# Optimization experiments

Measured on AMD Instinct MI355X. Metric: run time of the kernel, lower is better.

## Reference

```python
import jax, jax.numpy as jnp
import numpy as np

N, E = 30000, 240000          # nodes, edges per view
IN, D, OUT = 512, 128, 64      # in_dim, hidden_dim, out_dim
V, BLK, H, DM = 2, 2, 2, 64    # num_view, blk_size, num_heads, gate max-pool dim
NEG_ATT, NEG_OUT = 0.2, 0.01   # leaky_relu slopes (attention / outer)


def setup_inputs() -> dict:
    key = jax.random.key(0)
    ks = jax.random.split(key, 12)
    s = 0.05
    f32 = jnp.float32
    return {
        "ft": jax.random.normal(ks[0], (N, IN), f32),
        "src": jax.random.randint(ks[1], (V, E), 0, N, jnp.int32),
        "dst": jax.random.randint(ks[2], (V, E), 0, N, jnp.int32),
        "W_proj": jax.random.normal(ks[3], (IN, D), f32) * s,
        "W_embed": jax.random.normal(ks[4], (D, D), f32) * s,
        "a_l": jax.random.normal(ks[5], (V, BLK, H, D), f32) * s,
        "a_r": jax.random.normal(ks[6], (V, BLK, H, D), f32) * s,
        "Wv": jax.random.normal(ks[7], (V, BLK, H, D, D), f32) * s,
        "Wgm": jax.random.normal(ks[8], (V, BLK, D, DM), f32) * s,
        "Wgate": jax.random.normal(ks[9], (V, BLK, 2 * D + DM, H), f32) * s,
        "b_gate": jnp.zeros((V, BLK, H), f32),
        "W_tran": jax.random.normal(ks[10], (2 * D + DM and (D + V * H * D), OUT), f32) * s if False else jax.random.normal(ks[10], (D + V * H * D, OUT), f32) * s,
        "b_tran": jnp.zeros((OUT,), f32),
    }


def _seg_sum(x, idx):
    return jax.ops.segment_sum(x, idx, num_segments=N)


def _cgaan_layer(v, z, s_idx, d_idx, al, ar, wv, wgm, wgate, bg, merge):
    # v: [N,D] values, z: [N,D] attention features ('proj_z')
    # Multi-head attention logits: e_ij = leaky_relu(a_l.z_src + a_r.z_dst)  [E,H]
    logit_l = jnp.einsum("nd,hd->nh", z, al)
    logit_r = jnp.einsum("nd,hd->nh", z, ar)
    e = jax.nn.leaky_relu(logit_l[s_idx] + logit_r[d_idx], NEG_ATT)
    # edge softmax over incoming edges of each dst node
    m = jax.ops.segment_max(e, d_idx, num_segments=N)          # [N,H]
    ex = jnp.exp(e - m[d_idx])
    denom = _seg_sum(ex, d_idx)                                 # [N,H]
    alpha = ex / denom[d_idx]                                   # [E,H]
    # per-head value projection and weighted aggregation
    wvn = jnp.einsum("nd,hde->nhe", v, wv)                      # [N,H,D]
    agg = _seg_sum(alpha[:, :, None] * wvn[s_idx], d_idx)       # [N,H,D]
    # GaAN-style gate: sigmoid(FC([x_i, mean_j v_j, max_j (v_j Wgm)])) -> per-head scalar
    deg = _seg_sum(jnp.ones((s_idx.shape[0],), v.dtype), d_idx)  # [N]
    mean_n = _seg_sum(v[s_idx], d_idx) / jnp.maximum(deg, 1.0)[:, None]
    mx = jax.ops.segment_max((v @ wgm)[s_idx], d_idx, num_segments=N)
    mx = jnp.where(deg[:, None] > 0, mx, 0.0)                   # isolated nodes -> 0
    g = jax.nn.sigmoid(jnp.concatenate([v, mean_n, mx], -1) @ wgate + bg)  # [N,H]
    agg = g[:, :, None] * agg
    if merge == "mean":
        return agg.mean(axis=1)                                 # [N,D]
    return agg.reshape(agg.shape[0], -1)                        # cat -> [N,H*D]


def reference(ft, src, dst, W_proj, W_embed, a_l, a_r, Wv, Wgm, Wgate, b_gate, W_tran, b_tran):
    proj = ft @ W_proj                                          # [N,D]
    cur = [proj for _ in range(V)]
    for i in range(BLK):
        merge = "mean" if i < BLK - 1 else "cat"
        nxt = []
        for j in range(V):
            z = cur[j] @ W_embed
            h = _cgaan_layer(cur[j], z, src[j], dst[j], a_l[j, i], a_r[j, i],
                             Wv[j, i], Wgm[j, i], Wgate[j, i], b_gate[j, i], merge)
            nxt.append(jax.nn.leaky_relu(h, NEG_OUT))
        cur = nxt
    h = jnp.concatenate([proj] + cur, axis=-1)                  # [N, D+V*H*D]
    return h @ W_tran + b_tran
```

## Files before the change

### kernel.cpp

```cpp
#include <hip/hip_runtime.h>
#include <hip/hip_bf16.h>
#include <math.h>

#define NN 30000
#define EE 240000
#define IN_DIM 512
#define DD 128
#define OUTD 64
#define NV 2
#define NBLK 2
#define NH 2
#define DMM 64
#define NEG_ATT 0.2f
#define NEG_OUT 0.01f
#define CH 1024
#define NCH ((NN + CH - 1) / CH)

typedef __attribute__((ext_vector_type(8))) short bf16x8;
typedef __attribute__((ext_vector_type(4))) float f32x4;
typedef __attribute__((ext_vector_type(4))) unsigned short us4;
typedef __attribute__((ext_vector_type(8))) unsigned short us8;

#define OFF_PROJVM 0
#define OFF_WV     131072
#define OFF_WGM    262144
#define OFF_TRAN   278528
#define WT_TOTAL   319488

__device__ __forceinline__ unsigned short f2bf(float x) {
  unsigned u = __float_as_uint(x);
  return (unsigned short)((u + 0x7FFFu + ((u >> 16) & 1u)) >> 16);
}
__device__ __forceinline__ float bf2f(unsigned short u) {
  return __uint_as_float((unsigned)u << 16);
}
__device__ __forceinline__ void gload16(void* lds, const void* g) {
  __builtin_amdgcn_global_load_lds((const __attribute__((address_space(1))) unsigned int*)g,
                                   (__attribute__((address_space(3))) unsigned int*)lds, 16, 0, 0);
}

struct AUX {
  const int* fsrc; const int* fdst; const int* foff; int* fcur; int* fcsr;
  const unsigned short* lp0; const unsigned short* lp1; int lps;
  const float *lBl0, *lBr0, *lBl1, *lBr1, *lWg0, *lWg1;
  float4* llq; float2* llr;
};

__device__ void fill_body(int fb, int t, const AUX& a) {
  int e = fb * 256 + t;
  if (e >= NV * EE) return;
  int view = e / EE;
  int d = a.fdst[e];
  int p = atomicAdd(&a.fcur[view * NN + d], 1);
  a.fcsr[view * EE + a.foff[view * (NN + 1) + d] + p] = a.fsrc[e];
}

__device__ void llr_body(int lid, int t, const AUX& a) {
  int lane = t & 63, wid = t >> 6;
  int n = lid * 4 + wid;
  if (n >= NN) return;
  int k = lane * 2;
  unsigned av = *(const unsigned*)(a.lp0 + (size_t)n * a.lps + k);
  unsigned bv = *(const unsigned*)(a.lp1 + (size_t)n * a.lps + k);
  float ax = bf2f((unsigned short)av), ay = bf2f((unsigned short)(av >> 16));
  float bx = bf2f((unsigned short)bv), by = bf2f((unsigned short)(bv >> 16));
  float r[12];
  r[0]  = ax * a.lBl0[k * 2]     + ay * a.lBl0[k * 2 + 2];
  r[1]  = ax * a.lBl0[k * 2 + 1] + ay * a.lBl0[k * 2 + 3];
  r[2]  = ax * a.lBr0[k * 2]     + ay * a.lBr0[k * 2 + 2];
  r[3]  = ax * a.lBr0[k * 2 + 1] + ay * a.lBr0[k * 2 + 3];
  r[4]  = ax * a.lWg0[(128 + k) * 2]     + ay * a.lWg0[(129 + k) * 2];
  r[5]  = ax * a.lWg0[(128 + k) * 2 + 1] + ay * a.lWg0[(129 + k) * 2 + 1];
  r[6]  = bx * a.lBl1[k * 2]     + by * a.lBl1[k * 2 + 2];
  r[7]  = bx * a.lBl1[k * 2 + 1] + by * a.lBl1[k * 2 + 3];
  r[8]  = bx * a.lBr1[k * 2]     + by * a.lBr1[k * 2 + 2];
  r[9]  = bx * a.lBr1[k * 2 + 1] + by * a.lBr1[k * 2 + 3];
  r[10] = bx * a.lWg1[(128 + k) * 2]     + by * a.lWg1[(129 + k) * 2];
  r[11] = bx * a.lWg1[(128 + k) * 2 + 1] + by * a.lWg1[(129 + k) * 2 + 1];
  for (int s = 32; s; s >>= 1)
#pragma unroll
    for (int q = 0; q < 12; q++) r[q] += __shfl_xor(r[q], s);
  if (lane == 0) {
    a.llq[n] = make_float4(r[0], r[1], r[4], r[5]);
    a.llr[n] = make_float2(r[2], r[3]);
    a.llq[NN + n] = make_float4(r[6], r[7], r[10], r[11]);
    a.llr[NN + n] = make_float2(r[8], r[9]);
  }
}

__global__ __launch_bounds__(256) void kA_deg_prepw(const int* __restrict__ dst, int* __restrict__ deg,
                                                    const float* __restrict__ W_embed,
                                                    const float* __restrict__ a_l, const float* __restrict__ a_r,
                                                    const float* __restrict__ Wp, const float* __restrict__ Wgm,
                                                    float* __restrict__ Bl, float* __restrict__ Br,
                                                    float* __restrict__ wf) {
  int b = blockIdx.x;
  if (b < 1875) {
    int e = b * 256 + threadIdx.x;
    if (e < NV * EE) atomicAdd(&deg[(e / EE) * NN + dst[e]], 1);
    return;
  }
  int pb = b - 1875;
  if (pb < 256) {
    int idx = pb * 256 + threadIdx.x;
    int j = idx >> 15, k = (idx >> 6) & 511, n = idx & 63;
    const float* wp = Wp + (size_t)k * DD;
    const float* wg = Wgm + (size_t)(j * NBLK + 0) * DD * DMM + n;
    float s = 0.f;
    for (int e = 0; e < DD; e++) s += wp[e] * wg[(size_t)e * DMM];
    wf[idx] = s;
  } else {
    int idx = (pb - 256) * 256 + threadIdx.x;
    if (idx >= NV * NBLK * DD * NH) return;
    int h = idx & 1, dd = (idx >> 1) & 127, lv = idx >> 8;
    const float* w = W_embed + dd * DD;
    const float* al = a_l + (lv * NH + h) * DD;
    const float* ar = a_r + (lv * NH + h) * DD;
    float sl = 0.f, sr = 0.f;
    for (int e = 0; e < DD; e++) { float we = w[e]; sl += we * al[e]; sr += we * ar[e]; }
    Bl[idx] = sl; Br[idx] = sr;
  }
}

__global__ __launch_bounds__(256) void kB_scan1_wsplit(const int* __restrict__ deg, int* __restrict__ partial,
                                                       const float* __restrict__ Wp, const float* __restrict__ wf,
                                                       const float* __restrict__ Wv, const float* __restrict__ Wgm,
                                                       const float* __restrict__ Wt,
                                                       unsigned short* __restrict__ hi) {
  int b = blockIdx.x;
  if (b < 60) {
    int view = b / NCH, ch = b % NCH;
    const int* d = deg + view * NN + ch * CH;
    int rem = min(CH, NN - ch * CH);
    int t = threadIdx.x;
    int s = 0;
    for (int i = t; i < rem; i += 256) s += d[i];
    for (int k = 32; k; k >>= 1) s += __shfl_xor(s, k);
    __shared__ int wsum[4];
    if ((t & 63) == 0) wsum[t >> 6] = s;
    __syncthreads();
    if (t == 0) partial[b] = wsum[0] + wsum[1] + wsum[2] + wsum[3];
    return;
  }
  int wb = b - 60;
  const int pre[11] = {0, 256, 384, 512, 640, 768, 896, 1024, 1056, 1088, 1248};
  int y = 0;
  while (y < 10 && wb >= pre[y + 1]) y++;
  int bx = wb - pre[y];
  const float* src; int K, N; size_t doff;
  if (y == 0)      { src = Wp;                      K = 512; N = 128; doff = OFF_PROJVM; }
  else if (y <= 2) { int j = y - 1; src = wf + (size_t)j * 512 * 64; K = 512; N = 64; doff = OFF_PROJVM + (size_t)(128 + j * 64) * 512; }
  else if (y <= 6) { int lv = y - 3; src = Wv + (size_t)lv * 32768;  K = 256; N = 128; doff = OFF_WV + (size_t)lv * 32768; }
  else if (y <= 8) { int j = y - 7; src = Wgm + (size_t)(j * NBLK + 1) * 8192; K = 128; N = 64; doff = OFF_WGM + (size_t)j * 8192; }
  else             { src = Wt;                      K = 640; N = 64;  doff = OFF_TRAN; }
  int idx = bx * 256 + threadIdx.x;
  if (idx >= K * N) return;
  int n = idx / K, k = idx % K;
  int tk = k >> 6, g = (k >> 3) & 7, j2 = k & 7;
  int ks = (tk << 6) | ((g ^ (n & 7)) << 3) | j2;
  hi[doff + (size_t)n * K + ks] = f2bf(src[(size_t)k * N + n]);
}

__global__ __launch_bounds__(256) void k_scan3(const int* __restrict__ deg, const int* __restrict__ partial,
                                               int* __restrict__ off) {
  int b = blockIdx.x, view = b / NCH, ch = b % NCH;
  int coff = 0;
  for (int c = 0; c < ch; c++) coff += partial[view * NCH + c];
  int base = ch * CH;
  const int* d = deg + view * NN;
  int* o = off + view * (NN + 1);
  int t = threadIdx.x, lane = t & 63, w = t >> 6;
  int i0 = base + t * 4;
  int x0 = 0, x1 = 0, x2 = 0, x3 = 0;
  if (i0 + 3 < NN) { int4 q = *(const int4*)(d + i0); x0 = q.x; x1 = q.y; x2 = q.z; x3 = q.w; }
  else {
    if (i0     < NN) x0 = d[i0];
    if (i0 + 1 < NN) x1 = d[i0 + 1];
    if (i0 + 2 < NN) x2 = d[i0 + 2];
  }
  int tot = x0 + x1 + x2 + x3;
  int incl = tot;
  for (int k = 1; k < 64; k <<= 1) { int y = __shfl_up(incl, k); if (lane >= k) incl += y; }
  __shared__ int wt[4];
  if (lane == 63) wt[w] = incl;
  __syncthreads();
  int wexcl = 0;
  for (int k = 0; k < w; k++) wexcl += wt[k];
  int excl = coff + wexcl + incl - tot;
  if (i0     < NN) o[i0]     = excl;
  if (i0 + 1 < NN) o[i0 + 1] = excl + x0;
  if (i0 + 2 < NN) o[i0 + 2] = excl + x0 + x1;
  if (i0 + 3 < NN) o[i0 + 3] = excl + x0 + x1 + x2;
  if (ch == NCH - 1 && t == 0) o[NN] = coff + partial[b];
}

__global__ __launch_bounds__(256) void k_llr(AUX a) {
  llr_body(blockIdx.x, threadIdx.x, a);
}

__global__ __launch_bounds__(256) void k_edge(const int* __restrict__ off_, const int* __restrict__ csr_,
                                              const float4* __restrict__ lq_, const float2* __restrict__ lr_,
                                              const unsigned short* __restrict__ pk_, long viewStride,
                                              int ps, int vmoff0, int vmstep,
                                              const float* __restrict__ Wg_, const float* __restrict__ bg_,
                                              unsigned short* __restrict__ S_) {
  int view = blockIdx.y;
  const int* off = off_ + view * (NN + 1);
  const int* csr = csr_ + (size_t)view * EE;
  const float4* lq = lq_ + (size_t)view * NN;
  const float2* lrp = lr_ + (size_t)view * NN;
  const unsigned short* pk = pk_ + (size_t)view * viewStride;
  const char* pkc = (const char*)pk;
  int psb = ps * 2;
  int vmb = (vmoff0 + view * vmstep) * 2;
  const float* Wg = Wg_ + (size_t)view * NBLK * (2 * DD + DMM) * NH;
  const float* bg = bg_ + view * NBLK * NH;
  unsigned short* S = S_ + (size_t)view * NN * 256;

  int lane = threadIdx.x & 63, wid = threadIdx.x >> 6;
  int n = blockIdx.x * 4 + wid;
  int e0 = off[n], nb = off[n + 1] - e0;
  int half = lane >> 5, hl = lane & 31;
  if (nb == 0) {
    us4 z4 = {0, 0, 0, 0};
    *(us4*)(S + (size_t)n * 256 + half * 128 + 4 * hl) = z4;
    return;
  }
  float2 lrn = lrp[n];
  int voff = 8 * hl;
  int moff = vmb + 4 * hl;
  float sa0[4] = {0.f, 0.f, 0.f, 0.f}, sa1[4] = {0.f, 0.f, 0.f, 0.f};
  float d0 = 0.f, d1 = 0.f, tm0 = 0.f, tm1 = 0.f, vm0 = -INFINITY, vm1 = -INFINITY;
  for (int base = 0; base < nb; base += 64) {
    int i = base + lane;
    float w0 = 0.f, w1 = 0.f; unsigned boff = 0;
    if (i < nb) {
      int sidx = csr[e0 + i];
      boff = (unsigned)(sidx * psb);
      float4 qq = lq[sidx];
      float x0 = qq.x + lrn.x, x1 = qq.y + lrn.y;
      x0 = (x0 > 0.f) ? x0 : NEG_ATT * x0;
      x1 = (x1 > 0.f) ? x1 : NEG_ATT * x1;
      w0 = __expf(x0); w1 = __expf(x1);
      d0 += w0; d1 += w1; tm0 += qq.z; tm1 += qq.w;
    }
    int cnt = min(64, nb - base);
    int steps = (cnt + 1) >> 1;
    int j = half;
    unsigned bo = __shfl(boff, j);
    float wa = __shfl(w0, j), wb = __shfl(w1, j);
    us4 vq = *(const us4*)(pkc + bo + voff);
    unsigned mu = *(const unsigned*)(pkc + bo + moff);
    bool ok = (j < cnt);
    for (int s = 0; s < steps; s++) {
      int j1 = 2 * (s + 1) + half;
      int jc = min(j1, 63);
      unsigned bo1 = __shfl(boff, jc);
      float wa1 = __shfl(w0, jc), wb1 = __shfl(w1, jc);
      us4 vq1 = *(const us4*)(pkc + bo1 + voff);
      unsigned mu1 = *(const unsigned*)(pkc + bo1 + moff);
      float v0 = bf2f(vq[0]), v1 = bf2f(vq[1]), v2 = bf2f(vq[2]), v3 = bf2f(vq[3]);
      sa0[0] += wa * v0; sa0[1] += wa * v1; sa0[2] += wa * v2; sa0[3] += wa * v3;
      sa1[0] += wb * v0; sa1[1] += wb * v1; sa1[2] += wb * v2; sa1[3] += wb * v3;
      float mv0 = ok ? bf2f((unsigned short)mu) : -INFINITY;
      float mv1 = ok ? bf2f((unsigned short)(mu >> 16)) : -INFINITY;
      vm0 = fmaxf(vm0, mv0); vm1 = fmaxf(vm1, mv1);
      vq = vq1; mu = mu1; wa = wa1; wb = wb1; ok = (j1 < cnt);
    }
  }
#pragma unroll
  for (int k = 0; k < 4; k++) {
    sa0[k] += __shfl_xor(sa0[k], 32);
    sa1[k] += __shfl_xor(sa1[k], 32);
  }
  vm0 = fmaxf(vm0, __shfl_xor(vm0, 32));
  vm1 = fmaxf(vm1, __shfl_xor(vm1, 32));
  for (int s = 32; s; s >>= 1) { d0 += __shfl_xor(d0, s); d1 += __shfl_xor(d1, s); }
  unsigned vnu = *(const unsigned*)(pk + (size_t)n * ps + 2 * lane);
  float vnx = bf2f((unsigned short)vnu), vny = bf2f((unsigned short)(vnu >> 16));
  float im = 1.f / (float)nb;
  float p0 = vnx * Wg[(2 * lane) * 2]     + vny * Wg[(2 * lane + 1) * 2]     + tm0 * im;
  float p1 = vnx * Wg[(2 * lane) * 2 + 1] + vny * Wg[(2 * lane + 1) * 2 + 1] + tm1 * im;
  if (half == 1) {
    p0 += vm0 * Wg[(256 + 2 * hl) * 2]     + vm1 * Wg[(256 + 2 * hl + 1) * 2];
    p1 += vm0 * Wg[(256 + 2 * hl) * 2 + 1] + vm1 * Wg[(256 + 2 * hl + 1) * 2 + 1];
  }
  for (int s = 32; s; s >>= 1) { p0 += __shfl_xor(p0, s); p1 += __shfl_xor(p1, s); }
  float g0 = 1.f / (1.f + __expf(-(p0 + bg[0])));
  float g1 = 1.f / (1.f + __expf(-(p1 + bg[1])));
  float q0 = g0 / d0, q1 = g1 / d1;
  us4 o4;
  if (half == 0) {
    o4[0] = f2bf(sa0[0] * q0); o4[1] = f2bf(sa0[1] * q0);
    o4[2] = f2bf(sa0[2] * q0); o4[3] = f2bf(sa0[3] * q0);
  } else {
    o4[0] = f2bf(sa1[0] * q1); o4[1] = f2bf(sa1[1] * q1);
    o4[2] = f2bf(sa1[2] * q1); o4[3] = f2bf(sa1[3] * q1);
  }
  *(us4*)(S + (size_t)n * 256 + half * 128 + 4 * hl) = o4;
}

struct GB {
  const void* A[4];
  unsigned long long bofs[4];
  float* C[4];
  unsigned short* P[4];
  int ldc[4];
  int pldc[4];
};

template <int BN, int BM, bool ABF>
__global__ __launch_bounds__(256) void gemm_mfma(
    GB gb, AUX aux, const unsigned short* __restrict__ Bth,
    int lda, int ldb, int M, int K,
    const float* __restrict__ bias, float fs, int flags) {
  constexpr int NSUB = BN / 32;
  constexpr int CPW = BN / 32;
  constexpr int MS = BM / 32;
  __shared__ __align__(16) unsigned short Ah[BM][64];
  __shared__ __align__(16) unsigned short Bh[BN][64];
  int xb = blockIdx.x;
  const int z = blockIdx.z;
  if (flags & 8) {
    if (xb < 938) { fill_body(xb + 938 * z, threadIdx.x, aux); return; }
    xb -= 938;
  }
  if (flags & 16) {
    if (xb < 3750) { llr_body(xb + 3750 * z, threadIdx.x, aux); return; }
    xb -= 3750;
  }
  const float* __restrict__ Af = (const float*)gb.A[z];
  const unsigned short* __restrict__ Ab = (const unsigned short*)gb.A[z];
  float* __restrict__ C = gb.C[z];
  unsigned short* __restrict__ P = gb.P[z];
  const int ldc = gb.ldc[z], pldc = gb.pldc[z];
  const size_t bofs = gb.bofs[z];
  const int t = threadIdx.x;
  const int lane = t & 63, wv = t >> 6;
  const int lm = lane & 15, lg = lane >> 4;
  const int m0w = (wv & 1) * (BM / 2), n0w = (wv >> 1) * (BN / 2);
  const int row0 = xb * BM;
  f32x4 acc[MS][NSUB];
#pragma unroll
  for (int ms = 0; ms < MS; ms++)
#pragma unroll
    for (int ns = 0; ns < NSUB; ns++) acc[ms][ns] = (f32x4)0.f;

  float4 apre[MS][2];
  const int ar_ = t >> 3, ag_ = t & 7;

  auto loadA = [&](int k0) {
    if constexpr (!ABF) {
#pragma unroll
      for (int q = 0; q < MS; q++) {
        int rr = row0 + q * 32 + ar_;
        if (rr < M) {
          const float* p = Af + (size_t)rr * lda + k0 + ag_ * 8;
          apre[q][0] = *(const float4*)p;
          apre[q][1] = *(const float4*)(p + 4);
        } else {
          apre[q][0] = make_float4(0.f, 0.f, 0.f, 0.f);
          apre[q][1] = make_float4(0.f, 0.f, 0.f, 0.f);
        }
      }
    }
  };
  auto storeA = [&]() {
    if constexpr (!ABF) {
#pragma unroll
      for (int q = 0; q < MS; q++) {
        int r = q * 32 + ar_;
        us8 h8;
        float vals[8] = {apre[q][0].x, apre[q][0].y, apre[q][0].z, apre[q][0].w,
                         apre[q][1].x, apre[q][1].y, apre[q][1].z, apre[q][1].w};
#pragma unroll
        for (int e = 0; e < 8; e++) h8[e] = f2bf(vals[e]);
        int c = (ag_ ^ (r & 7)) << 3;
        *(us8*)&Ah[r][c] = h8;
      }
    }
  };
  auto stageA_bf = [&](int k0) {
    if constexpr (ABF) {
#pragma unroll
      for (int q = 0; q < MS; q++) {
        int r = q * 32 + ar_;
        int rr = min(row0 + r, M - 1);
        int scg = ag_ ^ (r & 7);
        gload16((char*)&Ah[0][0] + q * 4096 + t * 16,
                Ab + (size_t)rr * lda + k0 + scg * 8);
      }
    }
  };
  auto stageB = [&](int k0) {
#pragma unroll
    for (int q = 0; q < CPW; q++) {
      int chunk = wv * CPW + q;
      int o = chunk * 1024 + lane * 16;
      int n = o >> 7;
      int pq = (o >> 4) & 7;
      size_t gofs = bofs + (size_t)n * ldb + k0 + pq * 8;
      gload16((char*)&Bh[0][0] + o, Bth + gofs);
    }
  };

  loadA(0);
  for (int k0 = 0; k0 < K; k0 += 64) {
    if constexpr (ABF) stageA_bf(k0); else storeA();
    stageB(k0);
    __syncthreads();
    if constexpr (!ABF) { if (k0 + 64 < K) loadA(k0 + 64); }
#pragma unroll
    for (int kc = 0; kc < 2; kc++) {
      bf16x8 afh[MS], bfh[NSUB];
#pragma unroll
      for (int ms = 0; ms < MS; ms++) {
        int R = m0w + ms * 16 + lm;
        int c = (((kc * 4 + lg) ^ (R & 7)) << 3);
        afh[ms] = *(const bf16x8*)&Ah[R][c];
      }
#pragma unroll
      for (int ns = 0; ns < NSUB; ns++) {
        int R = n0w + ns * 16 + lm;
        int c = (((kc * 4 + lg) ^ (R & 7)) << 3);
        bfh[ns] = *(const bf16x8*)&Bh[R][c];
      }
#pragma unroll
      for (int ms = 0; ms < MS; ms++)
#pragma unroll
        for (int ns = 0; ns < NSUB; ns++)
          acc[ms][ns] = __builtin_amdgcn_mfma_f32_16x16x32_bf16(afh[ms], bfh[ns], acc[ms][ns], 0, 0, 0);
    }
    __syncthreads();
  }
#pragma unroll
  for (int ms = 0; ms < MS; ms++)
#pragma unroll
    for (int ns = 0; ns < NSUB; ns++)
#pragma unroll
      for (int j = 0; j < 4; j++) {
        int row = row0 + m0w + ms * 16 + lg * 4 + j;
        if (row >= M) continue;
        int col = n0w + ns * 16 + lm;
        float val = acc[ms][ns][j] * fs;
        if (bias) val += bias[col];
        if (flags & 2) val = (val > 0.f) ? val : NEG_OUT * val;
        if (C) C[(size_t)row * ldc + col] = val;
        if (P) P[(size_t)row * pldc + col] = f2bf(val);
      }
}

extern "C" void kernel_launch(void* const* d_in, const int* in_sizes, int n_in,
                              void* d_out, int out_size, void* d_ws, size_t ws_size,
                              hipStream_t stream) {
  const float* ft      = (const float*)d_in[0];
  const int*   src     = (const int*)  d_in[1];
  const int*   dst     = (const int*)  d_in[2];
  const float* W_proj  = (const float*)d_in[3];
  const float* W_embed = (const float*)d_in[4];
  const float* a_l     = (const float*)d_in[5];
  const float* a_r     = (const float*)d_in[6];
  const float* Wv      = (const float*)d_in[7];
  const float* Wgm     = (const float*)d_in[8];
  const float* Wgate   = (const float*)d_in[9];
  const float* b_gate  = (const float*)d_in[10];
  const float* W_tran  = (const float*)d_in[11];
  const float* b_tran  = (const float*)d_in[12];
  float* out = (float*)d_out;
  char* ws = (char*)d_ws;
  (void)in_sizes; (void)n_in; (void)out_size; (void)ws_size;

  size_t o = 0;
  auto take = [&](size_t bytes) { size_t r = o; o += (bytes + 255) & ~(size_t)255; return r; };
  int*   deg     = (int*)(ws + take((size_t)NV * NN * 4));
  int*   cursor  = (int*)(ws + take((size_t)NV * NN * 4));
  int*   csr_off = (int*)(ws + take((size_t)NV * (NN + 1) * 4));
  int*   csr_src = (int*)(ws + take((size_t)NV * EE * 4));
  int*   partial = (int*)(ws + take((size_t)NV * NCH * 4));
  float* Bl      = (float*)(ws + take((size_t)NV * NBLK * DD * NH * 4));
  float* Br      = (float*)(ws + take((size_t)NV * NBLK * DD * NH * 4));
  float* wf      = (float*)(ws + take((size_t)NV * 512 * 64 * 4));
  unsigned short* whi = (unsigned short*)(ws + take((size_t)WT_TOTAL * 2));
  float* h       = (float*)(ws + take((size_t)NN * 640 * 4));
  unsigned short* pk0 = (unsigned short*)(ws + take((size_t)NN * 256 * 2));
  unsigned short* pk1 = (unsigned short*)(ws + take((size_t)NV * NN * 192 * 2));
  unsigned short* Sbf = (unsigned short*)(ws + take((size_t)NV * NN * 256 * 2));
  float4* lqb    = (float4*)(ws + take((size_t)NV * NN * 16));
  float2* lrb    = (float2*)(ws + take((size_t)NV * NN * 8));

  const int HSTR = 640;
  const int GMB = (NN + 127) / 128;

  hipMemsetAsync(deg, 0, (size_t)(((size_t)NV * NN * 4 + 255) & ~(size_t)255) + (size_t)NV * NN * 4, stream);
  kA_deg_prepw<<<2135, 256, 0, stream>>>(dst, deg, W_embed, a_l, a_r, W_proj, Wgm, Bl, Br, wf);
  kB_scan1_wsplit<<<1308, 256, 0, stream>>>(deg, partial, W_proj, wf, Wv, Wgm, W_tran, whi);
  k_scan3<<<NV * NCH, 256, 0, stream>>>(deg, partial, csr_off);

  {
    GB gb = {};
    gb.A[0] = ft; gb.A[1] = ft;
    gb.bofs[0] = OFF_PROJVM; gb.bofs[1] = OFF_PROJVM + (size_t)128 * 512;
    gb.C[0] = h;  gb.ldc[0] = HSTR;
    gb.P[0] = pk0;       gb.pldc[0] = 256;
    gb.P[1] = pk0 + 128; gb.pldc[1] = 256;
    AUX ax = {};
    ax.fsrc = src; ax.fdst = dst; ax.foff = csr_off; ax.fcur = cursor; ax.fcsr = csr_src;
    gemm_mfma<128, 128, false><<<dim3(938 + GMB, 1, 2), 256, 0, stream>>>(gb, ax, whi, IN_DIM, 512,
                                                                          NN, 512, nullptr, 1.f, 8);
  }

  {
    AUX ax = {};
    ax.lp0 = pk0; ax.lp1 = pk0; ax.lps = 256;
    ax.lBl0 = Bl + 0 * 256; ax.lBr0 = Br + 0 * 256;
    ax.lBl1 = Bl + 2 * 256; ax.lBr1 = Br + 2 * 256;
    ax.lWg0 = Wgate; ax.lWg1 = Wgate + (size_t)NBLK * 320 * NH;
    ax.llq = lqb; ax.llr = lrb;
    k_llr<<<NN / 4, 256, 0, stream>>>(ax);
  }
  k_edge<<<dim3(NN / 4, 2), 256, 0, stream>>>(csr_off, csr_src, lqb, lrb,
                                              pk0, 0L, 256, 128, 64,
                                              Wgate, b_gate, Sbf);
  {
    GB gb = {};
    for (int j = 0; j < 2; j++) {
      gb.A[j] = Sbf + (size_t)j * NN * 256;
      gb.bofs[j] = OFF_WV + (size_t)(j * 2) * 32768;
      gb.P[j] = pk1 + (size_t)j * NN * 192;
      gb.pldc[j] = 192;
    }
    AUX ax = {};
    gemm_mfma<128, 128, true><<<dim3(GMB, 1, 2), 256, 0, stream>>>(gb, ax, whi, 256, 256, NN, 256,
                                                                   nullptr, 0.5f, 2);
  }
  {
    GB gb = {};
    for (int j = 0; j < 2; j++) {
      gb.A[j] = pk1 + (size_t)j * NN * 192;
      gb.bofs[j] = OFF_WGM + (size_t)j * 8192;
      gb.P[j] = pk1 + (size_t)j * NN * 192 + 128;
      gb.pldc[j] = 192;
    }
    AUX ax = {};
    ax.lp0 = pk1; ax.lp1 = pk1 + (size_t)NN * 192; ax.lps = 192;
    ax.lBl0 = Bl + 1 * 256; ax.lBr0 = Br + 1 * 256;
    ax.lBl1 = Bl + 3 * 256; ax.lBr1 = Br + 3 * 256;
    ax.lWg0 = Wgate + 640; ax.lWg1 = Wgate + (size_t)NBLK * 640 + 640;
    ax.llq = lqb; ax.llr = lrb;
    gemm_mfma<64, 128, true><<<dim3(3750 + GMB, 1, 2), 256, 0, stream>>>(gb, ax, whi, 192, 128,
                                                                         NN, 128, nullptr, 1.f, 16);
  }
  k_edge<<<dim3(NN / 4, 2), 256, 0, stream>>>(csr_off, csr_src, lqb, lrb,
                                              pk1, (long)NN * 192, 192, 128, 0,
                                              Wgate + 640, b_gate + NH, Sbf);
  {
    GB gb = {};
    for (int z = 0; z < 4; z++) {
      int j = z >> 1, hd = z & 1;
      gb.A[z] = Sbf + (size_t)j * NN * 256 + hd * 128;
      gb.bofs[z] = OFF_WV + (size_t)(j * 2 + 1) * 32768 + hd * 128;
      gb.C[z] = h + 128 + z * 128;
      gb.ldc[z] = HSTR;
    }
    AUX ax = {};
    gemm_mfma<128, 128, true><<<dim3(GMB, 1, 4), 256, 0, stream>>>(gb, ax, whi, 256, 256, NN, 128,
                                                                   nullptr, 1.f, 2);
  }
  {
    GB gb = {};
    gb.A[0] = h; gb.bofs[0] = OFF_TRAN; gb.C[0] = out; gb.ldc[0] = OUTD;
    AUX ax = {};
    gemm_mfma<64, 128, false><<<dim3(GMB, 1, 1), 256, 0, stream>>>(gb, ax, whi, HSTR, 640, NN, 640,
                                                                   b_tran, 1.f, 0);
  }
}
```

Measured before the change: 302.4 us.

## Fuse attention-logit reductions into GEMM epilogues and store concat buffer in bf16

Removes the standalone k_llr kernel and the llr_body blocks folded into the second-layer GEMM. The per-node logit and gate dot products are now computed in the epilogue of the GEMM that produces the features, reading the bf16 tile back from shared memory after a barrier. The concatenated h buffer changes from fp32 to bf16, which halves its write and read traffic in the final projection GEMM, and that GEMM now takes its input through the bf16 async-load path. The cost is extra epilogue work, shared-memory writes and a sync in the fused GEMMs, plus reduced precision in h.

```diff
diff --git a/kernel.cpp b/kernel.cpp
--- a/kernel.cpp
+++ b/kernel.cpp
@@ -41,7 +41,6 @@
 
 struct AUX {
   const int* fsrc; const int* fdst; const int* foff; int* fcur; int* fcsr;
-  const unsigned short* lp0; const unsigned short* lp1; int lps;
   const float *lBl0, *lBr0, *lBl1, *lBr1, *lWg0, *lWg1;
   float4* llq; float2* llr;
 };
@@ -53,39 +52,6 @@
   int d = a.fdst[e];
   int p = atomicAdd(&a.fcur[view * NN + d], 1);
   a.fcsr[view * EE + a.foff[view * (NN + 1) + d] + p] = a.fsrc[e];
-}
-
-__device__ void llr_body(int lid, int t, const AUX& a) {
-  int lane = t & 63, wid = t >> 6;
-  int n = lid * 4 + wid;
-  if (n >= NN) return;
-  int k = lane * 2;
-  unsigned av = *(const unsigned*)(a.lp0 + (size_t)n * a.lps + k);
-  unsigned bv = *(const unsigned*)(a.lp1 + (size_t)n * a.lps + k);
-  float ax = bf2f((unsigned short)av), ay = bf2f((unsigned short)(av >> 16));
-  float bx = bf2f((unsigned short)bv), by = bf2f((unsigned short)(bv >> 16));
-  float r[12];
-  r[0]  = ax * a.lBl0[k * 2]     + ay * a.lBl0[k * 2 + 2];
-  r[1]  = ax * a.lBl0[k * 2 + 1] + ay * a.lBl0[k * 2 + 3];
-  r[2]  = ax * a.lBr0[k * 2]     + ay * a.lBr0[k * 2 + 2];
-  r[3]  = ax * a.lBr0[k * 2 + 1] + ay * a.lBr0[k * 2 + 3];
-  r[4]  = ax * a.lWg0[(128 + k) * 2]     + ay * a.lWg0[(129 + k) * 2];
-  r[5]  = ax * a.lWg0[(128 + k) * 2 + 1] + ay * a.lWg0[(129 + k) * 2 + 1];
-  r[6]  = bx * a.lBl1[k * 2]     + by * a.lBl1[k * 2 + 2];
-  r[7]  = bx * a.lBl1[k * 2 + 1] + by * a.lBl1[k * 2 + 3];
-  r[8]  = bx * a.lBr1[k * 2]     + by * a.lBr1[k * 2 + 2];
-  r[9]  = bx * a.lBr1[k * 2 + 1] + by * a.lBr1[k * 2 + 3];
-  r[10] = bx * a.lWg1[(128 + k) * 2]     + by * a.lWg1[(129 + k) * 2];
-  r[11] = bx * a.lWg1[(128 + k) * 2 + 1] + by * a.lWg1[(129 + k) * 2 + 1];
-  for (int s = 32; s; s >>= 1)
-#pragma unroll
-    for (int q = 0; q < 12; q++) r[q] += __shfl_xor(r[q], s);
-  if (lane == 0) {
-    a.llq[n] = make_float4(r[0], r[1], r[4], r[5]);
-    a.llr[n] = make_float2(r[2], r[3]);
-    a.llq[NN + n] = make_float4(r[6], r[7], r[10], r[11]);
-    a.llr[NN + n] = make_float2(r[8], r[9]);
-  }
 }
 
 __global__ __launch_bounds__(256) void kA_deg_prepw(const int* __restrict__ dst, int* __restrict__ deg,
@@ -192,10 +158,6 @@
   if (i0 + 2 < NN) o[i0 + 2] = excl + x0 + x1;
   if (i0 + 3 < NN) o[i0 + 3] = excl + x0 + x1 + x2;
   if (ch == NCH - 1 && t == 0) o[NN] = coff + partial[b];
-}
-
-__global__ __launch_bounds__(256) void k_llr(AUX a) {
-  llr_body(blockIdx.x, threadIdx.x, a);
 }
 
 __global__ __launch_bounds__(256) void k_edge(const int* __restrict__ off_, const int* __restrict__ csr_,
@@ -305,11 +267,13 @@
   unsigned long long bofs[4];
   float* C[4];
   unsigned short* P[4];
+  unsigned short* P2[4];
   int ldc[4];
   int pldc[4];
+  int p2ldc[4];
 };
 
-template <int BN, int BM, bool ABF>
+template <int BN, int BM, bool ABF, int EPI>
 __global__ __launch_bounds__(256) void gemm_mfma(
     GB gb, AUX aux, const unsigned short* __restrict__ Bth,
     int lda, int ldb, int M, int K,
@@ -317,23 +281,19 @@
   constexpr int NSUB = BN / 32;
   constexpr int CPW = BN / 32;
   constexpr int MS = BM / 32;
-  __shared__ __align__(16) unsigned short Ah[BM][64];
-  __shared__ __align__(16) unsigned short Bh[BN][64];
+  __shared__ __align__(16) unsigned short SMEM[BM * 64 + BN * 64];
   int xb = blockIdx.x;
   const int z = blockIdx.z;
   if (flags & 8) {
     if (xb < 938) { fill_body(xb + 938 * z, threadIdx.x, aux); return; }
     xb -= 938;
   }
-  if (flags & 16) {
-    if (xb < 3750) { llr_body(xb + 3750 * z, threadIdx.x, aux); return; }
-    xb -= 3750;
-  }
   const float* __restrict__ Af = (const float*)gb.A[z];
   const unsigned short* __restrict__ Ab = (const unsigned short*)gb.A[z];
   float* __restrict__ C = gb.C[z];
   unsigned short* __restrict__ P = gb.P[z];
-  const int ldc = gb.ldc[z], pldc = gb.pldc[z];
+  unsigned short* __restrict__ P2 = gb.P2[z];
+  const int ldc = gb.ldc[z], pldc = gb.pldc[z], p2ldc = gb.p2ldc[z];
   const size_t bofs = gb.bofs[z];
   const int t = threadIdx.x;
   const int lane = t & 63, wv = t >> 6;
@@ -376,7 +336,7 @@
 #pragma unroll
         for (int e = 0; e < 8; e++) h8[e] = f2bf(vals[e]);
         int c = (ag_ ^ (r & 7)) << 3;
-        *(us8*)&Ah[r][c] = h8;
+        *(us8*)&SMEM[r * 64 + c] = h8;
       }
     }
   };
@@ -387,7 +347,7 @@
         int r = q * 32 + ar_;
         int rr = min(row0 + r, M - 1);
         int scg = ag_ ^ (r & 7);
-        gload16((char*)&Ah[0][0] + q * 4096 + t * 16,
+        gload16((char*)&SMEM[0] + q * 4096 + t * 16,
                 Ab + (size_t)rr * lda + k0 + scg * 8);
       }
     }
@@ -400,7 +360,7 @@
       int n = o >> 7;
       int pq = (o >> 4) & 7;
       size_t gofs = bofs + (size_t)n * ldb + k0 + pq * 8;
-      gload16((char*)&Bh[0][0] + o, Bth + gofs);
+      gload16((char*)&SMEM[BM * 64] + o, Bth + gofs);
     }
   };
 
@@ -417,13 +377,13 @@
       for (int ms = 0; ms < MS; ms++) {
         int R = m0w + ms * 16 + lm;
         int c = (((kc * 4 + lg) ^ (R & 7)) << 3);
-        afh[ms] = *(const bf16x8*)&Ah[R][c];
+        afh[ms] = *(const bf16x8*)&SMEM[R * 64 + c];
       }
 #pragma unroll
       for (int ns = 0; ns < NSUB; ns++) {
         int R = n0w + ns * 16 + lm;
         int c = (((kc * 4 + lg) ^ (R & 7)) << 3);
-        bfh[ns] = *(const bf16x8*)&Bh[R][c];
+        bfh[ns] = *(const bf16x8*)&SMEM[BM * 64 + R * 64 + c];
       }
 #pragma unroll
       for (int ms = 0; ms < MS; ms++)
@@ -439,15 +399,71 @@
     for (int ns = 0; ns < NSUB; ns++)
 #pragma unroll
       for (int j = 0; j < 4; j++) {
-        int row = row0 + m0w + ms * 16 + lg * 4 + j;
-        if (row >= M) continue;
+        int r = m0w + ms * 16 + lg * 4 + j;
+        int row = row0 + r;
         int col = n0w + ns * 16 + lm;
         float val = acc[ms][ns][j] * fs;
         if (bias) val += bias[col];
         if (flags & 2) val = (val > 0.f) ? val : NEG_OUT * val;
-        if (C) C[(size_t)row * ldc + col] = val;
-        if (P) P[(size_t)row * pldc + col] = f2bf(val);
-      }
+        unsigned short bv = f2bf(val);
+        if constexpr (EPI != 0) {
+          int p = col >> 6, cc = col & 63, g = cc >> 3, jj = cc & 7;
+          SMEM[p * (BM * 64) + r * 64 + (((g ^ (r & 7)) << 3) | jj)] = bv;
+        }
+        if (row < M) {
+          if (C) C[(size_t)row * ldc + col] = val;
+          if (P) P[(size_t)row * pldc + col] = bv;
+          if (P2) P2[(size_t)row * p2ldc + col] = bv;
+        }
+      }
+  if constexpr (EPI != 0) {
+    if (EPI == 2 || z == 0) {
+      __syncthreads();
+      const float* vBl = (EPI == 2 && z) ? aux.lBl1 : aux.lBl0;
+      const float* vBr = (EPI == 2 && z) ? aux.lBr1 : aux.lBr0;
+      const float* vWg = (EPI == 2 && z) ? aux.lWg1 : aux.lWg0;
+      float4 cb0 = *(const float4*)(vBl + 4 * lane);
+      float4 cr0 = *(const float4*)(vBr + 4 * lane);
+      float4 cg0 = *(const float4*)(vWg + 256 + 4 * lane);
+      float4 cb1, cr1, cg1;
+      if constexpr (EPI == 1) {
+        cb1 = *(const float4*)(aux.lBl1 + 4 * lane);
+        cr1 = *(const float4*)(aux.lBr1 + 4 * lane);
+        cg1 = *(const float4*)(aux.lWg1 + 256 + 4 * lane);
+      }
+      int pp = lane >> 5, cc = (2 * lane) & 63, gg = cc >> 3, jj2 = cc & 7;
+      for (int i = 0; i < BM / 4; i++) {
+        int r = wv * (BM / 4) + i;
+        int n = row0 + r;
+        unsigned u = *(const unsigned*)&SMEM[pp * (BM * 64) + r * 64 + (((gg ^ (r & 7)) << 3) | jj2)];
+        float ax = bf2f((unsigned short)u), ay = bf2f((unsigned short)(u >> 16));
+        float rv[12];
+        rv[0] = ax * cb0.x + ay * cb0.z;  rv[1] = ax * cb0.y + ay * cb0.w;
+        rv[2] = ax * cr0.x + ay * cr0.z;  rv[3] = ax * cr0.y + ay * cr0.w;
+        rv[4] = ax * cg0.x + ay * cg0.z;  rv[5] = ax * cg0.y + ay * cg0.w;
+        if constexpr (EPI == 1) {
+          rv[6]  = ax * cb1.x + ay * cb1.z;  rv[7]  = ax * cb1.y + ay * cb1.w;
+          rv[8]  = ax * cr1.x + ay * cr1.z;  rv[9]  = ax * cr1.y + ay * cr1.w;
+          rv[10] = ax * cg1.x + ay * cg1.z;  rv[11] = ax * cg1.y + ay * cg1.w;
+        }
+        constexpr int NR = (EPI == 1) ? 12 : 6;
+        for (int s = 32; s; s >>= 1)
+#pragma unroll
+          for (int q = 0; q < NR; q++) rv[q] += __shfl_xor(rv[q], s);
+        if (lane == 0 && n < NN) {
+          if constexpr (EPI == 1) {
+            aux.llq[n] = make_float4(rv[0], rv[1], rv[4], rv[5]);
+            aux.llr[n] = make_float2(rv[2], rv[3]);
+            aux.llq[NN + n] = make_float4(rv[6], rv[7], rv[10], rv[11]);
+            aux.llr[NN + n] = make_float2(rv[8], rv[9]);
+          } else {
+            aux.llq[(size_t)z * NN + n] = make_float4(rv[0], rv[1], rv[4], rv[5]);
+            aux.llr[(size_t)z * NN + n] = make_float2(rv[2], rv[3]);
+          }
+        }
+      }
+    }
+  }
 }
 
 extern "C" void kernel_launch(void* const* d_in, const int* in_sizes, int n_in,
@@ -481,14 +497,13 @@
   float* Br      = (float*)(ws + take((size_t)NV * NBLK * DD * NH * 4));
   float* wf      = (float*)(ws + take((size_t)NV * 512 * 64 * 4));
   unsigned short* whi = (unsigned short*)(ws + take((size_t)WT_TOTAL * 2));
-  float* h       = (float*)(ws + take((size_t)NN * 640 * 4));
+  unsigned short* hb  = (unsigned short*)(ws + take((size_t)NN * 640 * 2));
   unsigned short* pk0 = (unsigned short*)(ws + take((size_t)NN * 256 * 2));
   unsigned short* pk1 = (unsigned short*)(ws + take((size_t)NV * NN * 192 * 2));
   unsigned short* Sbf = (unsigned short*)(ws + take((size_t)NV * NN * 256 * 2));
   float4* lqb    = (float4*)(ws + take((size_t)NV * NN * 16));
   float2* lrb    = (float2*)(ws + take((size_t)NV * NN * 8));
 
-  const int HSTR = 640;
   const int GMB = (NN + 127) / 128;
 
   hipMemsetAsync(deg, 0, (size_t)(((size_t)NV * NN * 4 + 255) & ~(size_t)255) + (size_t)NV * NN * 4, stream);
@@ -500,23 +515,16 @@
     GB gb = {};
     gb.A[0] = ft; gb.A[1] = ft;
     gb.bofs[0] = OFF_PROJVM; gb.bofs[1] = OFF_PROJVM + (size_t)128 * 512;
-    gb.C[0] = h;  gb.ldc[0] = HSTR;
-    gb.P[0] = pk0;       gb.pldc[0] = 256;
-    gb.P[1] = pk0 + 128; gb.pldc[1] = 256;
+    gb.P[0] = pk0;        gb.pldc[0] = 256;
+    gb.P2[0] = hb;        gb.p2ldc[0] = 640;
+    gb.P[1] = pk0 + 128;  gb.pldc[1] = 256;
     AUX ax = {};
     ax.fsrc = src; ax.fdst = dst; ax.foff = csr_off; ax.fcur = cursor; ax.fcsr = csr_src;
-    gemm_mfma<128, 128, false><<<dim3(938 + GMB, 1, 2), 256, 0, stream>>>(gb, ax, whi, IN_DIM, 512,
-                                                                          NN, 512, nullptr, 1.f, 8);
-  }
-
-  {
-    AUX ax = {};
-    ax.lp0 = pk0; ax.lp1 = pk0; ax.lps = 256;
-    ax.lBl0 = Bl + 0 * 256; ax.lBr0 = Br + 0 * 256;
-    ax.lBl1 = Bl + 2 * 256; ax.lBr1 = Br + 2 * 256;
-    ax.lWg0 = Wgate; ax.lWg1 = Wgate + (size_t)NBLK * 320 * NH;
+    ax.lBl0 = Bl + 0 * 256; ax.lBr0 = Br + 0 * 256; ax.lWg0 = Wgate;
+    ax.lBl1 = Bl + 2 * 256; ax.lBr1 = Br + 2 * 256; ax.lWg1 = Wgate + (size_t)NBLK * 320 * NH;
     ax.llq = lqb; ax.llr = lrb;
-    k_llr<<<NN / 4, 256, 0, stream>>>(ax);
+    gemm_mfma<128, 128, false, 1><<<dim3(938 + GMB, 1, 2), 256, 0, stream>>>(gb, ax, whi, IN_DIM, 512,
+                                                                             NN, 512, nullptr, 1.f, 8);
   }
   k_edge<<<dim3(NN / 4, 2), 256, 0, stream>>>(csr_off, csr_src, lqb, lrb,
                                               pk0, 0L, 256, 128, 64,
@@ -530,8 +538,11 @@
       gb.pldc[j] = 192;
     }
     AUX ax = {};
-    gemm_mfma<128, 128, true><<<dim3(GMB, 1, 2), 256, 0, stream>>>(gb, ax, whi, 256, 256, NN, 256,
-                                                                   nullptr, 0.5f, 2);
+    ax.lBl0 = Bl + 1 * 256; ax.lBr0 = Br + 1 * 256; ax.lWg0 = Wgate + 640;
+    ax.lBl1 = Bl + 3 * 256; ax.lBr1 = Br + 3 * 256; ax.lWg1 = Wgate + (size_t)NBLK * 640 + 640;
+    ax.llq = lqb; ax.llr = lrb;
+    gemm_mfma<128, 128, true, 2><<<dim3(GMB, 1, 2), 256, 0, stream>>>(gb, ax, whi, 256, 256, NN, 256,
+                                                                      nullptr, 0.5f, 2);
   }
   {
     GB gb = {};
@@ -542,13 +553,8 @@
       gb.pldc[j] = 192;
     }
     AUX ax = {};
-    ax.lp0 = pk1; ax.lp1 = pk1 + (size_t)NN * 192; ax.lps = 192;
-    ax.lBl0 = Bl + 1 * 256; ax.lBr0 = Br + 1 * 256;
-    ax.lBl1 = Bl + 3 * 256; ax.lBr1 = Br + 3 * 256;
-    ax.lWg0 = Wgate + 640; ax.lWg1 = Wgate + (size_t)NBLK * 640 + 640;
-    ax.llq = lqb; ax.llr = lrb;
-    gemm_mfma<64, 128, true><<<dim3(3750 + GMB, 1, 2), 256, 0, stream>>>(gb, ax, whi, 192, 128,
-                                                                         NN, 128, nullptr, 1.f, 16);
+    gemm_mfma<64, 128, true, 0><<<dim3(GMB, 1, 2), 256, 0, stream>>>(gb, ax, whi, 192, 128,
+                                                                     NN, 128, nullptr, 1.f, 0);
   }
   k_edge<<<dim3(NN / 4, 2), 256, 0, stream>>>(csr_off, csr_src, lqb, lrb,
                                               pk1, (long)NN * 192, 192, 128, 0,
@@ -559,18 +565,18 @@
       int j = z >> 1, hd = z & 1;
       gb.A[z] = Sbf + (size_t)j * NN * 256 + hd * 128;
       gb.bofs[z] = OFF_WV + (size_t)(j * 2 + 1) * 32768 + hd * 128;
-      gb.C[z] = h + 128 + z * 128;
-      gb.ldc[z] = HSTR;
+      gb.P[z] = hb + 128 + z * 128;
+      gb.pldc[z] = 640;
     }
     AUX ax = {};
-    gemm_mfma<128, 128, true><<<dim3(GMB, 1, 4), 256, 0, stream>>>(gb, ax, whi, 256, 256, NN, 128,
-                                                                   nullptr, 1.f, 2);
+    gemm_mfma<128, 128, true, 0><<<dim3(GMB, 1, 4), 256, 0, stream>>>(gb, ax, whi, 256, 256, NN, 128,
+                                                                      nullptr, 1.f, 2);
   }
   {
     GB gb = {};
-    gb.A[0] = h; gb.bofs[0] = OFF_TRAN; gb.C[0] = out; gb.ldc[0] = OUTD;
+    gb.A[0] = hb; gb.bofs[0] = OFF_TRAN; gb.C[0] = out; gb.ldc[0] = OUTD;
     AUX ax = {};
-    gemm_mfma<64, 128, false><<<dim3(GMB, 1, 1), 256, 0, stream>>>(gb, ax, whi, HSTR, 640, NN, 640,
-                                                                   b_tran, 1.f, 0);
-  }
-}
+    gemm_mfma<64, 128, true, 0><<<dim3(GMB, 1, 1), 256, 0, stream>>>(gb, ax, whi, 640, 640, NN, 640,
+                                                                     b_tran, 1.f, 0);
+  }
+}
```

New measurement: 340.4 us. +12.6%, slower.
